# Performance work log

Measured on AMD Instinct MI355X. Metric: run time of the kernel, lower is better.

## Reference

```python
import jax, jax.numpy as jnp
import numpy as np

B, L, D = 4, 2048, 512
H = 8
DH = D // H  # 64
SCALE = DH // H  # faithful to source: key.size(-1)//num_heads = 64//8 = 8 (multiplicative)
LN_EPS = 1e-5


def setup_inputs() -> dict:
    key = jax.random.key(0)
    ks = jax.random.split(key, 16)
    s = 1.0 / np.sqrt(D)
    inp = {
        "query": jax.random.normal(ks[0], (B, L, D), jnp.float32),
        "key": jax.random.normal(ks[1], (B, L, D), jnp.float32),
        "value": jax.random.normal(ks[2], (B, L, D), jnp.float32),
        "Wq": jax.random.uniform(ks[3], (D, D), jnp.float32, -s, s),
        "bq": jax.random.uniform(ks[4], (D,), jnp.float32, -s, s),
        "Wk": jax.random.uniform(ks[5], (D, D), jnp.float32, -s, s),
        "bk": jax.random.uniform(ks[6], (D,), jnp.float32, -s, s),
        "Wv": jax.random.uniform(ks[7], (D, D), jnp.float32, -s, s),
        "bv": jax.random.uniform(ks[8], (D,), jnp.float32, -s, s),
        "Wo": jax.random.uniform(ks[9], (D, D), jnp.float32, -s, s),
        "bo": jax.random.uniform(ks[10], (D,), jnp.float32, -s, s),
        "gamma": jnp.ones((D,), jnp.float32),
        "beta": jnp.zeros((D,), jnp.float32),
    }
    return inp


def _layer_norm(x, gamma, beta):
    mu = jnp.mean(x, axis=-1, keepdims=True)
    var = jnp.mean(jnp.square(x - mu), axis=-1, keepdims=True)
    return (x - mu) * jax.lax.rsqrt(var + LN_EPS) * gamma + beta


def reference(query, key, value, Wq, bq, Wk, bk, Wv, bv, Wo, bo, gamma, beta):
    res = query
    # QKV projections: [B, L, D]
    q = query @ Wq.T + bq
    k = key @ Wk.T + bk
    v = value @ Wv.T + bv
    # faithful to source: raw view(B*H, -1, DH) with NO transpose
    q = q.reshape(B * H, -1, DH)
    k = k.reshape(B * H, -1, DH)
    v = v.reshape(B * H, -1, DH)
    # bmm -> multiplicative scale -> softmax(dim=2) -> bmm
    attn = jnp.einsum('bqd,bkd->bqk', q, k) * SCALE  # [B*H, L, L]
    attn = jax.nn.softmax(attn, axis=2)
    ctx = jnp.einsum('bqk,bkd->bqd', attn, v)        # [B*H, L, DH]
    ctx = ctx.reshape(B, -1, DH * H)                  # [B, L, D]
    out = ctx @ Wo.T + bo
    out = _layer_norm(res + out, gamma, beta)
    return (out, attn)
```

## Files before the change

kernel.cpp:

```cpp
#include <hip/hip_runtime.h>

#define LSEQ 2048
#define DMODEL 512
#define DHD 64
#define SLAB (LSEQ*DHD)

typedef __attribute__((ext_vector_type(8))) short short8;
typedef __attribute__((ext_vector_type(4))) float f32x4;
typedef float f4raw __attribute__((ext_vector_type(4)));
typedef _Float16 half8 __attribute__((ext_vector_type(8)));
typedef _Float16 h4_t  __attribute__((ext_vector_type(4)));

__device__ __forceinline__ short f2bf(float x) {
    union { float f; unsigned u; } v; v.f = x;
    unsigned r = v.u + 0x7FFF + ((v.u >> 16) & 1);
    return (short)(r >> 16);
}
__device__ __forceinline__ float bf2f(short h) {
    union { float f; unsigned u; } v; v.u = ((unsigned)(unsigned short)h) << 16;
    return v.f;
}

#define GLOAD_LDS16(g, l) __builtin_amdgcn_global_load_lds( \
    (const __attribute__((address_space(1))) void*)(g),     \
    (__attribute__((address_space(3))) void*)(l), 16, 0, 0)

#define VMCNT0()  asm volatile("s_waitcnt vmcnt(0)" ::: "memory")
#define VMCNT2()  asm volatile("s_waitcnt vmcnt(2)" ::: "memory")
#define VMCNT4()  asm volatile("s_waitcnt vmcnt(4)" ::: "memory")
#define LGKM0()   asm volatile("s_waitcnt lgkmcnt(0)" ::: "memory")
#define SCHEDB()  __builtin_amdgcn_sched_barrier(0)
#define BARRIER() do { __builtin_amdgcn_s_barrier(); __builtin_amdgcn_sched_barrier(0); } while (0)

template<int MODE>
__global__ __launch_bounds__(256) void proj_gemm(
    const float* __restrict__ A, const float* __restrict__ W,
    const float* __restrict__ bias, float* __restrict__ Cf,
    short* __restrict__ C0)
{
    __shared__ __align__(16) short Ah[64][40], Al[64][40], Bh[64][40], Bl[64][40];

    const int tid  = threadIdx.x;
    const int lane = tid & 63, wv = tid >> 6;
    const int wm = wv >> 1, wn = wv & 1;
    const int fr = lane & 15, kg = lane >> 4;
    const int m0 = blockIdx.y * 64, n0 = blockIdx.x * 64;

    f32x4 acc[2][2];
    #pragma unroll
    for (int i = 0; i < 2; ++i)
        #pragma unroll
        for (int j = 0; j < 2; ++j) { f32x4 z = {0.f,0.f,0.f,0.f}; acc[i][j] = z; }

    const int srow = tid >> 2, sc8 = (tid & 3) << 3;

    for (int kt = 0; kt < 16; ++kt) {
        __syncthreads();
        {
            const float* ap = A + (size_t)(m0 + srow) * DMODEL + kt*32 + sc8;
            float4 a0 = *(const float4*)ap;
            float4 a1 = *(const float4*)(ap + 4);
            float va[8] = {a0.x,a0.y,a0.z,a0.w,a1.x,a1.y,a1.z,a1.w};
            short8 h, l;
            #pragma unroll
            for (int j = 0; j < 8; ++j) { short hh = f2bf(va[j]); h[j] = hh; l[j] = f2bf(va[j] - bf2f(hh)); }
            *(short8*)&Ah[srow][sc8] = h; *(short8*)&Al[srow][sc8] = l;

            const float* wp = W + (size_t)(n0 + srow) * DMODEL + kt*32 + sc8;
            float4 b0 = *(const float4*)wp;
            float4 b1 = *(const float4*)(wp + 4);
            float vb[8] = {b0.x,b0.y,b0.z,b0.w,b1.x,b1.y,b1.z,b1.w};
            #pragma unroll
            for (int j = 0; j < 8; ++j) { short hh = f2bf(vb[j]); h[j] = hh; l[j] = f2bf(vb[j] - bf2f(hh)); }
            *(short8*)&Bh[srow][sc8] = h; *(short8*)&Bl[srow][sc8] = l;
        }
        __syncthreads();

        short8 ah[2], al[2], bh[2], bl[2];
        #pragma unroll
        for (int mf = 0; mf < 2; ++mf) {
            ah[mf] = *(short8*)&Ah[wm*32 + mf*16 + fr][kg*8];
            al[mf] = *(short8*)&Al[wm*32 + mf*16 + fr][kg*8];
        }
        #pragma unroll
        for (int nf = 0; nf < 2; ++nf) {
            bh[nf] = *(short8*)&Bh[wn*32 + nf*16 + fr][kg*8];
            bl[nf] = *(short8*)&Bl[wn*32 + nf*16 + fr][kg*8];
        }
        #pragma unroll
        for (int mf = 0; mf < 2; ++mf)
            #pragma unroll
            for (int nf = 0; nf < 2; ++nf) {
                acc[mf][nf] = __builtin_amdgcn_mfma_f32_16x16x32_bf16(ah[mf], bh[nf], acc[mf][nf], 0,0,0);
                acc[mf][nf] = __builtin_amdgcn_mfma_f32_16x16x32_bf16(ah[mf], bl[nf], acc[mf][nf], 0,0,0);
                acc[mf][nf] = __builtin_amdgcn_mfma_f32_16x16x32_bf16(al[mf], bh[nf], acc[mf][nf], 0,0,0);
            }
    }

    #pragma unroll
    for (int mf = 0; mf < 2; ++mf)
        #pragma unroll
        for (int nf = 0; nf < 2; ++nf) {
            const int col = n0 + wn*32 + nf*16 + fr;
            const float bv = bias[col];
            #pragma unroll
            for (int r = 0; r < 4; ++r) {
                const int row = m0 + wm*32 + mf*16 + kg*4 + r;
                const float o = acc[mf][nf][r] + bv;
                const size_t idx = (size_t)row * DMODEL + col;
                if (MODE == 0) Cf[idx] = o;
                else           ((_Float16*)C0)[idx] = (_Float16)o;
            }
        }
}

__global__ __launch_bounds__(256) void vtransf_kernel(
    const short* __restrict__ vh, short* __restrict__ vtf)
{
    __shared__ short T[64][72];
    const int tid = threadIdx.x;
    const int s  = blockIdx.y;
    const int t0 = blockIdx.x * 64;
    const size_t slab = (size_t)s * SLAB;

    {
        const int r = tid >> 2, c0 = (tid & 3) << 4;
        const short* src = vh + slab + (size_t)(t0 + r) * DHD + c0;
        short8 a = *(const short8*)src;
        short8 b = *(const short8*)(src + 8);
        *(short8*)&T[r][c0]     = a;
        *(short8*)&T[r][c0 + 8] = b;
    }
    __syncthreads();
    {
        const int kbl = tid >> 6, d = tid & 63;
        short8 o0, o1;
        #pragma unroll
        for (int j = 0; j < 8; ++j) { o0[j] = T[kbl*16 + j][d]; o1[j] = T[kbl*16 + 8 + j][d]; }
        short* dst = vtf + slab + ((size_t)((t0 >> 4) + kbl) * 64 + d) * 16;
        *(short8*)dst       = o0;
        *(short8*)(dst + 8) = o1;
    }
}

__global__ __launch_bounds__(512, 4) void attn_kernel(
    const _Float16* __restrict__ qf, const _Float16* __restrict__ kf,
    const _Float16* __restrict__ vtf,
    float* __restrict__ attn, float* __restrict__ ctx)
{
    __shared__ __align__(16) char KBuf[49152];
    __shared__ float redA[8][16];
    __shared__ float mrow[16], lirow[16];

    const int tid  = threadIdx.x;
    const int lane = tid & 63, wv = tid >> 6;
    const int fr = lane & 15, kg = lane >> 4;

    const int wg  = blockIdx.x;
    const int rem = wg & 1023;
    const int q0  = (rem >> 3) << 4;
    const int bh  = ((wg >> 10) << 3) + (rem & 7);
    const size_t slab = (size_t)bh * SLAB;

    half8 qa[2];
    #pragma unroll
    for (int ks = 0; ks < 2; ++ks)
        qa[ks] = *(const half8*)(qf + slab + (size_t)(q0 + fr) * DHD + ks*32 + kg*8);

    const int srow = lane >> 3;
    const int scb  = (lane & 7) ^ srow;

    f32x4 s[16];

    #define STAGE_K(TI, CUR) { \
        _Pragma("unroll") \
        for (int j = 0; j < 2; ++j) { \
            const int b = wv*2 + j; \
            GLOAD_LDS16(kf + slab + (size_t)((TI)*128 + b*8 + srow)*DHD + scb*8, \
                        KBuf + (CUR)*16384 + b*1024); \
        } }

    STAGE_K(0, 0);
    STAGE_K(1, 1);

    const int klo = (wv << 4) + fr;
    const int sw  = fr & 7;
    #pragma unroll
    for (int i = 0; i < 16; ++i) {
        if (i + 2 < 16) {
            SCHEDB();
            LGKM0();
            STAGE_K(i + 2, (i + 2) % 3);
        }

        if      (i <= 13) VMCNT4();
        else if (i == 14) VMCNT2();
        else              VMCNT0();

        const char* rp = KBuf + (i % 3)*16384 + (klo << 7);
        half8 kb0 = *(const half8*)(rp + ((kg ^ sw) << 4));
        half8 kb1 = *(const half8*)(rp + (((4 + kg) ^ sw) << 4));

        f32x4 a = {0.f,0.f,0.f,0.f};
        a = __builtin_amdgcn_mfma_f32_16x16x32_f16(kb0, qa[0], a, 0,0,0);
        a = __builtin_amdgcn_mfma_f32_16x16x32_f16(kb1, qa[1], a, 0,0,0);
        s[i] = a;
    }
    #undef STAGE_K

    float m;
    {
        f32x4 mx = s[0];
        #pragma unroll
        for (int i = 1; i < 16; ++i) {
            mx.x = fmaxf(mx.x, s[i].x); mx.y = fmaxf(mx.y, s[i].y);
            mx.z = fmaxf(mx.z, s[i].z); mx.w = fmaxf(mx.w, s[i].w);
        }
        m = fmaxf(fmaxf(mx.x, mx.y), fmaxf(mx.z, mx.w));
        m = fmaxf(m, __shfl_xor(m, 16));
        m = fmaxf(m, __shfl_xor(m, 32));
    }
    if (lane < 16) redA[wv][lane] = m;
    __syncthreads();
    if (tid < 16) {
        float mm = redA[0][tid];
        #pragma unroll
        for (int w = 1; w < 8; ++w) mm = fmaxf(mm, redA[w][tid]);
        mrow[tid] = mm;
    }
    __syncthreads();
    m = mrow[fr];

    const float C = 8.0f * 1.44269504089f;
    float sum = 0.f;
    #pragma unroll
    for (int i = 0; i < 16; ++i) {
        f32x4 p;
        p.x = exp2f((s[i].x - m) * C);
        p.y = exp2f((s[i].y - m) * C);
        p.z = exp2f((s[i].z - m) * C);
        p.w = exp2f((s[i].w - m) * C);
        s[i] = p;
        sum += (p.x + p.y) + (p.z + p.w);
    }
    sum += __shfl_xor(sum, 16);
    sum += __shfl_xor(sum, 32);
    if (lane < 16) redA[wv][lane] = sum;
    __syncthreads();
    if (tid < 16) {
        float l = 0.f;
        #pragma unroll
        for (int w = 0; w < 8; ++w) l += redA[w][tid];
        lirow[tid] = 1.0f / l;
    }
    __syncthreads();
    const float li = lirow[fr];

    f32x4 acc[4];
    #pragma unroll
    for (int db = 0; db < 4; ++db) { f32x4 z = {0.f,0.f,0.f,0.f}; acc[db] = z; }

    _Float16* PBh = (_Float16*)KBuf;
    const _Float16* vfb = vtf + slab;
    const int sq = tid >> 5, sc = tid & 31;
    float* abase = attn + ((size_t)bh * LSEQ + q0 + sq) * LSEQ + (sc << 2);

    int cur = 0;
    #pragma unroll
    for (int t = 0; t < 16; ++t) {
        f32x4 p = s[t];
        p.x *= li; p.y *= li; p.z *= li; p.w *= li;
        h4_t pw = { (_Float16)p.x, (_Float16)p.y, (_Float16)p.z, (_Float16)p.w };

        *(h4_t*)&PBh[(size_t)cur*2176 + fr*136 + (wv << 4) + (kg << 2)] = pw;

        const _Float16* vb = vfb + ((size_t)(t*8 + wv) << 10) + (fr << 4) + (kg << 2);
        #pragma unroll
        for (int db = 0; db < 4; ++db) {
            h4_t va = *(const h4_t*)(vb + db*256);
            acc[db] = __builtin_amdgcn_mfma_f32_16x16x16f16(va, pw, acc[db], 0,0,0);
        }

        LGKM0();
        BARRIER();

        h4_t pr = *(const h4_t*)&PBh[(size_t)cur*2176 + sq*136 + (sc << 2)];
        f4raw o = { (float)pr[0], (float)pr[1], (float)pr[2], (float)pr[3] };
        __builtin_nontemporal_store(o, (f4raw*)(abase + (size_t)t * 128));

        cur ^= 1;
    }

    __syncthreads();
    {
        float* pt = (float*)KBuf;
        #pragma unroll
        for (int db = 0; db < 4; ++db) {
            float4 o = { acc[db].x, acc[db].y, acc[db].z, acc[db].w };
            *(float4*)(pt + wv*1024 + fr*64 + db*16 + (kg << 2)) = o;
        }
    }
    __syncthreads();
    {
        float* pt = (float*)KBuf;
        const int e = tid << 1;
        const int q = e >> 6, d = e & 63;
        float2 r2 = {0.f, 0.f};
        #pragma unroll
        for (int w = 0; w < 8; ++w) {
            float2 t2 = *(float2*)(pt + w*1024 + q*64 + d);
            r2.x += t2.x; r2.y += t2.y;
        }
        *(float2*)(ctx + slab + (size_t)(q0 + q) * DHD + d) = r2;
    }
}

__global__ __launch_bounds__(128) void ln_kernel(
    const float* __restrict__ resid, const float* __restrict__ x,
    const float* __restrict__ gamma, const float* __restrict__ beta,
    float* __restrict__ out)
{
    const int row = blockIdx.x;
    const int tid = threadIdx.x;
    const size_t base = (size_t)row * DMODEL + tid*4;

    float4 v = *(const float4*)(x + base);
    float4 rq = *(const float4*)(resid + base);
    v.x += rq.x; v.y += rq.y; v.z += rq.z; v.w += rq.w;

    float s  = v.x + v.y + v.z + v.w;
    float ss = v.x*v.x + v.y*v.y + v.z*v.z + v.w*v.w;
    #pragma unroll
    for (int d = 1; d < 64; d <<= 1) { s += __shfl_xor(s, d); ss += __shfl_xor(ss, d); }

    __shared__ float red[2][2];
    const int wv = tid >> 6;
    if ((tid & 63) == 0) { red[wv][0] = s; red[wv][1] = ss; }
    __syncthreads();
    s  = red[0][0] + red[1][0];
    ss = red[0][1] + red[1][1];

    const float mu  = s * (1.0f/512.0f);
    const float var = ss * (1.0f/512.0f) - mu*mu;
    const float rs  = rsqrtf(var + 1e-5f);

    float4 g = *(const float4*)(gamma + tid*4);
    float4 b = *(const float4*)(beta + tid*4);
    float4 o;
    o.x = (v.x - mu) * rs * g.x + b.x;
    o.y = (v.y - mu) * rs * g.y + b.y;
    o.z = (v.z - mu) * rs * g.z + b.z;
    o.w = (v.w - mu) * rs * g.w + b.w;
    *(float4*)(out + base) = o;
}

extern "C" void kernel_launch(void* const* d_in, const int* in_sizes, int n_in,
                              void* d_out, int out_size, void* d_ws, size_t ws_size,
                              hipStream_t stream)
{
    const float* query = (const float*)d_in[0];
    const float* key   = (const float*)d_in[1];
    const float* value = (const float*)d_in[2];
    const float* Wq = (const float*)d_in[3];
    const float* bq = (const float*)d_in[4];
    const float* Wk = (const float*)d_in[5];
    const float* bk = (const float*)d_in[6];
    const float* Wv = (const float*)d_in[7];
    const float* bv = (const float*)d_in[8];
    const float* Wo = (const float*)d_in[9];
    const float* bo = (const float*)d_in[10];
    const float* gamma = (const float*)d_in[11];
    const float* beta  = (const float*)d_in[12];

    float* out  = (float*)d_out;
    float* attn = out + 4194304;

    const size_t NTOK = (size_t)8192 * 512;
    short* qv = (short*)d_ws;
    short* kv = qv + NTOK;
    short* vf = kv + NTOK;
    short* vtf = vf + NTOK;
    float* obuf = (float*)d_ws;

    dim3 pgrid(8, 128), pblk(256);
    proj_gemm<3><<<pgrid, pblk, 0, stream>>>(query, Wq, bq, nullptr, qv);
    proj_gemm<3><<<pgrid, pblk, 0, stream>>>(key,   Wk, bk, nullptr, kv);
    proj_gemm<3><<<pgrid, pblk, 0, stream>>>(value, Wv, bv, nullptr, vf);

    vtransf_kernel<<<dim3(32, 32), 256, 0, stream>>>(vf, vtf);

    attn_kernel<<<4096, 512, 0, stream>>>((const _Float16*)qv, (const _Float16*)kv,
                                          (const _Float16*)vtf, attn, out );

    proj_gemm<0><<<pgrid, pblk, 0, stream>>>(out , Wo, bo, obuf, nullptr);
    ln_kernel<<<8192, 128, 0, stream>>>(query, obuf, gamma, beta, out);
}
```

Before: 286.3 us.

## Pre-split weights into bf16 hi/lo fragment layout and batch QKV projections

Adds a kernel that converts all four weight matrices once per call into bf16 hi/lo pairs stored in an MFMA-fragment-ordered layout. The projection GEMM then reads weight fragments straight from global memory, with no LDS staging and no per-tile conversion. Each block now covers a wider 64x256 tile with 512 threads, so the activation conversion is shared across more output columns. The three QKV projections are merged into one launch through grid z. The trade-off is an extra launch and workspace for the converted weights, plus uncoalesced-style global fragment loads in place of shared-memory reuse.

```diff
diff --git a/kernel.cpp b/kernel.cpp
--- a/kernel.cpp
+++ b/kernel.cpp
@@ -6,6 +6,7 @@
 #define SLAB (LSEQ*DHD)
 
 typedef __attribute__((ext_vector_type(8))) short short8;
+typedef __attribute__((ext_vector_type(4))) short short4v;
 typedef __attribute__((ext_vector_type(4))) float f32x4;
 typedef float f4raw __attribute__((ext_vector_type(4)));
 typedef _Float16 half8 __attribute__((ext_vector_type(8)));
@@ -32,86 +33,113 @@
 #define SCHEDB()  __builtin_amdgcn_sched_barrier(0)
 #define BARRIER() do { __builtin_amdgcn_s_barrier(); __builtin_amdgcn_sched_barrier(0); } while (0)
 
+__global__ __launch_bounds__(256) void convw_kernel(
+    const float* __restrict__ W0, const float* __restrict__ W1,
+    const float* __restrict__ W2, const float* __restrict__ W3,
+    short* __restrict__ F0, short* __restrict__ F1,
+    short* __restrict__ F2, short* __restrict__ F3)
+{
+    const int which = blockIdx.y;
+    const float* W = which==0 ? W0 : which==1 ? W1 : which==2 ? W2 : W3;
+    short*       F = which==0 ? F0 : which==1 ? F1 : which==2 ? F2 : F3;
+
+    const int g  = blockIdx.x * 256 + threadIdx.x;
+    const int n  = g >> 6, kc = g & 63;
+    const float* src = W + (size_t)n * 512 + kc * 8;
+    float4 a0 = *(const float4*)src;
+    float4 a1 = *(const float4*)(src + 4);
+    float v[8] = {a0.x,a0.y,a0.z,a0.w,a1.x,a1.y,a1.z,a1.w};
+    short8 h, l;
+    #pragma unroll
+    for (int j = 0; j < 8; ++j) { short hh = f2bf(v[j]); h[j] = hh; l[j] = f2bf(v[j] - bf2f(hh)); }
+
+    const int nt = n >> 4, fr = n & 15, kt = kc >> 2, kg = kc & 3;
+    short* dh = F + ((size_t)(nt*16 + kt) * 2) * 512 + fr*32 + kg*8;
+    *(short8*)dh        = h;
+    *(short8*)(dh + 512) = l;
+}
+
 template<int MODE>
-__global__ __launch_bounds__(256) void proj_gemm(
-    const float* __restrict__ A, const float* __restrict__ W,
-    const float* __restrict__ bias, float* __restrict__ Cf,
-    short* __restrict__ C0)
-{
-    __shared__ __align__(16) short Ah[64][40], Al[64][40], Bh[64][40], Bl[64][40];
+__global__ __launch_bounds__(512) void proj2_kernel(
+    const float* __restrict__ A0, const float* __restrict__ A1, const float* __restrict__ A2,
+    const short* __restrict__ F0, const short* __restrict__ F1, const short* __restrict__ F2,
+    const float* __restrict__ b0, const float* __restrict__ b1, const float* __restrict__ b2,
+    float* __restrict__ Cf0, float* __restrict__ Cf1, float* __restrict__ Cf2,
+    short* __restrict__ C00, short* __restrict__ C01, short* __restrict__ C02)
+{
+    __shared__ __align__(16) short Ah[64][40], Al[64][40];
+
+    const int z = blockIdx.z;
+    const float* A    = z==0 ? A0 : z==1 ? A1 : A2;
+    const short* F    = z==0 ? F0 : z==1 ? F1 : F2;
+    const float* bias = z==0 ? b0 : z==1 ? b1 : b2;
+    float* Cf         = z==0 ? Cf0 : z==1 ? Cf1 : Cf2;
+    short* C0         = z==0 ? C00 : z==1 ? C01 : C02;
 
     const int tid  = threadIdx.x;
     const int lane = tid & 63, wv = tid >> 6;
-    const int wm = wv >> 1, wn = wv & 1;
     const int fr = lane & 15, kg = lane >> 4;
-    const int m0 = blockIdx.y * 64, n0 = blockIdx.x * 64;
-
-    f32x4 acc[2][2];
-    #pragma unroll
-    for (int i = 0; i < 2; ++i)
-        #pragma unroll
-        for (int j = 0; j < 2; ++j) { f32x4 z = {0.f,0.f,0.f,0.f}; acc[i][j] = z; }
-
-    const int srow = tid >> 2, sc8 = (tid & 3) << 3;
+    const int m0 = blockIdx.y * 64, n0 = blockIdx.x * 256;
+
+    f32x4 acc[4][2];
+    #pragma unroll
+    for (int i = 0; i < 4; ++i)
+        #pragma unroll
+        for (int j = 0; j < 2; ++j) { f32x4 zo = {0.f,0.f,0.f,0.f}; acc[i][j] = zo; }
+
+    const int srow = tid >> 3, sc4 = (tid & 7) << 2;
 
     for (int kt = 0; kt < 16; ++kt) {
         __syncthreads();
         {
-            const float* ap = A + (size_t)(m0 + srow) * DMODEL + kt*32 + sc8;
+            const float* ap = A + (size_t)(m0 + srow) * DMODEL + kt*32 + sc4;
             float4 a0 = *(const float4*)ap;
-            float4 a1 = *(const float4*)(ap + 4);
-            float va[8] = {a0.x,a0.y,a0.z,a0.w,a1.x,a1.y,a1.z,a1.w};
-            short8 h, l;
+            float v[4] = {a0.x, a0.y, a0.z, a0.w};
+            short4v h, l;
             #pragma unroll
-            for (int j = 0; j < 8; ++j) { short hh = f2bf(va[j]); h[j] = hh; l[j] = f2bf(va[j] - bf2f(hh)); }
-            *(short8*)&Ah[srow][sc8] = h; *(short8*)&Al[srow][sc8] = l;
-
-            const float* wp = W + (size_t)(n0 + srow) * DMODEL + kt*32 + sc8;
-            float4 b0 = *(const float4*)wp;
-            float4 b1 = *(const float4*)(wp + 4);
-            float vb[8] = {b0.x,b0.y,b0.z,b0.w,b1.x,b1.y,b1.z,b1.w};
+            for (int j = 0; j < 4; ++j) { short hh = f2bf(v[j]); h[j] = hh; l[j] = f2bf(v[j] - bf2f(hh)); }
+            *(short4v*)&Ah[srow][sc4] = h;
+            *(short4v*)&Al[srow][sc4] = l;
+        }
+        __syncthreads();
+
+        short8 ah[4], al[4];
+        #pragma unroll
+        for (int mf = 0; mf < 4; ++mf) {
+            ah[mf] = *(short8*)&Ah[mf*16 + fr][kg*8];
+            al[mf] = *(short8*)&Al[mf*16 + fr][kg*8];
+        }
+        #pragma unroll
+        for (int nf = 0; nf < 2; ++nf) {
+            const int nt = (n0 >> 4) + wv*2 + nf;
+            const short* wf = F + ((size_t)(nt*16 + kt) * 2) * 512 + fr*32 + kg*8;
+            short8 wh = *(const short8*)wf;
+            short8 wl = *(const short8*)(wf + 512);
             #pragma unroll
-            for (int j = 0; j < 8; ++j) { short hh = f2bf(vb[j]); h[j] = hh; l[j] = f2bf(vb[j] - bf2f(hh)); }
-            *(short8*)&Bh[srow][sc8] = h; *(short8*)&Bl[srow][sc8] = l;
-        }
-        __syncthreads();
-
-        short8 ah[2], al[2], bh[2], bl[2];
-        #pragma unroll
-        for (int mf = 0; mf < 2; ++mf) {
-            ah[mf] = *(short8*)&Ah[wm*32 + mf*16 + fr][kg*8];
-            al[mf] = *(short8*)&Al[wm*32 + mf*16 + fr][kg*8];
-        }
-        #pragma unroll
-        for (int nf = 0; nf < 2; ++nf) {
-            bh[nf] = *(short8*)&Bh[wn*32 + nf*16 + fr][kg*8];
-            bl[nf] = *(short8*)&Bl[wn*32 + nf*16 + fr][kg*8];
-        }
-        #pragma unroll
-        for (int mf = 0; mf < 2; ++mf)
-            #pragma unroll
-            for (int nf = 0; nf < 2; ++nf) {
-                acc[mf][nf] = __builtin_amdgcn_mfma_f32_16x16x32_bf16(ah[mf], bh[nf], acc[mf][nf], 0,0,0);
-                acc[mf][nf] = __builtin_amdgcn_mfma_f32_16x16x32_bf16(ah[mf], bl[nf], acc[mf][nf], 0,0,0);
-                acc[mf][nf] = __builtin_amdgcn_mfma_f32_16x16x32_bf16(al[mf], bh[nf], acc[mf][nf], 0,0,0);
+            for (int mf = 0; mf < 4; ++mf) {
+                acc[mf][nf] = __builtin_amdgcn_mfma_f32_16x16x32_bf16(ah[mf], wh, acc[mf][nf], 0,0,0);
+                acc[mf][nf] = __builtin_amdgcn_mfma_f32_16x16x32_bf16(ah[mf], wl, acc[mf][nf], 0,0,0);
+                acc[mf][nf] = __builtin_amdgcn_mfma_f32_16x16x32_bf16(al[mf], wh, acc[mf][nf], 0,0,0);
             }
-    }
-
-    #pragma unroll
-    for (int mf = 0; mf < 2; ++mf)
-        #pragma unroll
-        for (int nf = 0; nf < 2; ++nf) {
-            const int col = n0 + wn*32 + nf*16 + fr;
-            const float bv = bias[col];
+        }
+    }
+
+    #pragma unroll
+    for (int nf = 0; nf < 2; ++nf) {
+        const int col = n0 + wv*32 + nf*16 + fr;
+        const float bv = bias[col];
+        #pragma unroll
+        for (int mf = 0; mf < 4; ++mf) {
             #pragma unroll
             for (int r = 0; r < 4; ++r) {
-                const int row = m0 + wm*32 + mf*16 + kg*4 + r;
+                const int row = m0 + mf*16 + kg*4 + r;
                 const float o = acc[mf][nf][r] + bv;
                 const size_t idx = (size_t)row * DMODEL + col;
                 if (MODE == 0) Cf[idx] = o;
                 else           ((_Float16*)C0)[idx] = (_Float16)o;
             }
         }
+    }
 }
 
 __global__ __launch_bounds__(256) void vtransf_kernel(
@@ -380,18 +408,26 @@
     short* kv = qv + NTOK;
     short* vf = kv + NTOK;
     short* vtf = vf + NTOK;
+    short* wfq = vtf + NTOK;
+    short* wfk = wfq + 524288;
+    short* wfv = wfk + 524288;
+    short* wfo = wfv + 524288;
     float* obuf = (float*)d_ws;
 
-    dim3 pgrid(8, 128), pblk(256);
-    proj_gemm<3><<<pgrid, pblk, 0, stream>>>(query, Wq, bq, nullptr, qv);
-    proj_gemm<3><<<pgrid, pblk, 0, stream>>>(key,   Wk, bk, nullptr, kv);
-    proj_gemm<3><<<pgrid, pblk, 0, stream>>>(value, Wv, bv, nullptr, vf);
+    convw_kernel<<<dim3(128, 4), 256, 0, stream>>>(Wq, Wk, Wv, Wo, wfq, wfk, wfv, wfo);
+
+    proj2_kernel<3><<<dim3(2, 128, 3), 512, 0, stream>>>(
+        query, key, value, wfq, wfk, wfv, bq, bk, bv,
+        nullptr, nullptr, nullptr, qv, kv, vf);
 
     vtransf_kernel<<<dim3(32, 32), 256, 0, stream>>>(vf, vtf);
 
     attn_kernel<<<4096, 512, 0, stream>>>((const _Float16*)qv, (const _Float16*)kv,
                                           (const _Float16*)vtf, attn, out );
 
-    proj_gemm<0><<<pgrid, pblk, 0, stream>>>(out , Wo, bo, obuf, nullptr);
+    proj2_kernel<0><<<dim3(2, 128, 1), 512, 0, stream>>>(
+        out , out, out, wfo, wfo, wfo, bo, bo, bo,
+        obuf, obuf, obuf, nullptr, nullptr, nullptr);
+
     ln_kernel<<<8192, 128, 0, stream>>>(query, obuf, gamma, beta, out);
 }
```

Result: faster. 248.7 us (-13.1%).
